# Kernel optimization log

Hardware: AMD Instinct MI355X
Metric: run time of the kernel (lower is better)

The kernel has to match this reference:

```python
import jax, jax.numpy as jnp
import numpy as np
from jax import lax

# channel-gather index lists for the 16 c3 branches (from the torch source)
IDX3 = np.array([0,1,2, 1,2,3, 2,3,4, 3,4,5, 0,4,5, 0,1,5])          # 6 branches x 3 ch
IDX4 = np.array([0,1,2,3, 1,2,3,4, 2,3,4,5, 0,3,4,5, 0,1,4,5,
                 0,1,2,5, 0,1,3,4, 1,2,4,5, 0,2,3,5])                  # 9 branches x 4 ch
F6_SCALE = 1.7519


def _conv(x, w, groups=1):
    # NCHW x OIHW, stride 1, VALID padding (all convs in the model)
    return lax.conv_general_dilated(x, w, (1, 1), 'VALID', feature_group_count=groups)


def _avgpool2(x):
    return lax.reduce_window(x, 0.0, lax.add, (1, 1, 2, 2), (1, 1, 2, 2), 'VALID') * 0.25


def _bconv(x, w, b, groups=1):
    # BinaryConvFunction.forward: sign(conv(sign(x), sign(w)) + b)
    out = _conv(jnp.sign(x), jnp.sign(w), groups) + b[None, :, None, None]
    return jnp.sign(out)


def setup_inputs() -> dict:
    key = jax.random.key(0)
    ks = jax.random.split(key, 16)
    B = 8192
    return {
        'x':     jax.random.normal(ks[0], (B, 1, 32, 32), jnp.float32),
        'c1_w':  jax.random.normal(ks[1], (6, 1, 5, 5), jnp.float32) * 0.2,
        'c1_b':  jax.random.normal(ks[2], (6,), jnp.float32) * 0.1,
        'w3':    jax.random.normal(ks[3], (6, 3, 5, 5), jnp.float32),   # 6 grouped 3-ch branches
        'b3':    jax.random.normal(ks[4], (6,), jnp.float32) * 0.1,
        'w4':    jax.random.normal(ks[5], (9, 4, 5, 5), jnp.float32),   # 9 grouped 4-ch branches
        'b4':    jax.random.normal(ks[6], (9,), jnp.float32) * 0.1,
        'w6':    jax.random.normal(ks[7], (1, 6, 5, 5), jnp.float32),   # 1 branch on all 6 ch
        'b6':    jax.random.normal(ks[8], (1,), jnp.float32) * 0.1,
        'c5_w':  jax.random.normal(ks[9], (120, 16, 5, 5), jnp.float32),
        'c5_b':  jax.random.normal(ks[10], (120,), jnp.float32) * 0.1,
        'f6_w':  jax.random.normal(ks[11], (84, 120), jnp.float32) * 0.1,
        'f6_b':  jax.random.normal(ks[12], (84,), jnp.float32) * 0.1,
        'rbf_w': jax.random.normal(ks[13], (10, 84), jnp.float32) * 0.1,
        'rbf_b': jax.random.normal(ks[14], (10,), jnp.float32) * 0.1,
    }


def reference(x, c1_w, c1_b, w3, b3, w4, b4, w6, b6, c5_w, c5_b, f6_w, f6_b, rbf_w, rbf_b):
    # c1 (full-precision conv) + relu + s2 avgpool: [B,1,32,32] -> [B,6,14,14]
    h = _avgpool2(jax.nn.relu(_conv(x, c1_w) + c1_b[None, :, None, None]))
    # 16 binary branch convs, batched as grouped convs over gathered channels
    o3 = _bconv(h[:, IDX3], w3, b3, groups=6)   # [B,6,10,10]
    o4 = _bconv(h[:, IDX4], w4, b4, groups=9)   # [B,9,10,10]
    o6 = _bconv(h, w6, b6)                      # [B,1,10,10]
    h = jnp.concatenate([o3, o4, o6], axis=1)   # [B,16,10,10] (matches torch cat order)
    h = _avgpool2(jax.nn.relu(h))               # [B,16,5,5]
    h = _bconv(h, c5_w, c5_b)                   # [B,120,1,1]
    h = h.reshape(h.shape[0], -1)               # [B,120]
    h = jnp.tanh((h @ f6_w.T + f6_b) * F6_SCALE)
    return jax.nn.relu(h @ rbf_w.T + rbf_b)     # [B,10]
```

## Files before the change

kernel.cpp:

```cpp
#include <hip/hip_runtime.h>
#include <stdint.h>

typedef float v2f __attribute__((ext_vector_type(2)));

constexpr int IDX3[18] = {0,1,2, 1,2,3, 2,3,4, 3,4,5, 0,4,5, 0,1,5};
constexpr int IDX4[36] = {0,1,2,3, 1,2,3,4, 2,3,4,5, 0,3,4,5, 0,1,4,5,
                          0,1,2,5, 0,1,3,4, 1,2,4,5, 0,2,3,5};


__global__ void prepack_kernel(const float* __restrict__ w3, const float* __restrict__ w4,
                               const float* __restrict__ w6, const float* __restrict__ c5w,
                               unsigned* __restrict__ ws) {
    int t = blockIdx.x * blockDim.x + threadIdx.x;
    if (t < 60) {
        const float* src = (t < 18) ? (w3 + t * 25)
                          : (t < 54) ? (w4 + (t - 18) * 25)
                          : (w6 + (t - 54) * 25);
        unsigned m = 0;
        for (int p = 0; p < 25; ++p) if (src[p] > 0.f) m |= 1u << p;
        ws[t] = m;
    } else if (t < 1620) {
        int q = t - 60, oc = q / 13, w = q % 13;
        unsigned m = 0;
        for (int b = 0; b < 32; ++b) {
            int g = w * 32 + b;
            int qi = g >> 4, ic = g & 15;
            if (qi < 25 && c5w[oc * 400 + ic * 25 + qi] > 0.f) m |= 1u << b;
        }
        ws[60 + q] = m;
    }
}

__global__ __launch_bounds__(256, 4) void lenet_fused(
    const float* __restrict__ x, const float* __restrict__ c1w, const float* __restrict__ c1b,
    const float* __restrict__ b3, const float* __restrict__ b4, const float* __restrict__ b6,
    const float* __restrict__ c5b, const unsigned* __restrict__ ws,
    const float* __restrict__ f6w, const float* __restrict__ f6b,
    const float* __restrict__ rbfw, const float* __restrict__ rbfb,
    float* __restrict__ out, int B) {
    __shared__ float wS[150];
    __shared__ float bS[6], b3S[6], b4S[9], b6S[1];
    __shared__ unsigned hrow[3][6][14];
    __shared__ unsigned sbits[3][100];
    __shared__ unsigned c5in[3][13];
    __shared__ float4 sS4[3][30];
    __shared__ float f6o[3][84];

    const int t = threadIdx.x;
    const int img0 = blockIdx.x * 3;
    const int nimg = min(3, B - img0);

    if (t < 150) wS[t] = c1w[t];
    if (t < 6) { bS[t] = c1b[t]; b3S[t] = b3[t]; }
    if (t < 9) b4S[t] = b4[t];
    if (t == 0) b6S[0] = b6[0];
    __syncthreads();

    if (t < nimg * 84) {
        const int denom = nimg * 6;
        int py = t / denom, rem = t % denom, img = rem / 6, c = rem % 6;
        float wr[25];
        #pragma unroll
        for (int i = 0; i < 25; ++i) wr[i] = wS[c * 25 + i];
        const float bias = bS[c];
        v2f accp[28];
        #pragma unroll
        for (int j = 0; j < 28; ++j) accp[j] = (v2f){bias, bias};
        const float* xp = x + (size_t)(img0 + img) * 1024 + (2 * py) * 32;
        #pragma unroll
        for (int r = 0; r < 6; ++r) {
            float rv[32];
            #pragma unroll
            for (int q = 0; q < 8; ++q) {
                float4 v = ((const float4*)(xp + r * 32))[q];
                rv[4 * q] = v.x; rv[4 * q + 1] = v.y; rv[4 * q + 2] = v.z; rv[4 * q + 3] = v.w;
            }
            if (r == 0) {
                #pragma unroll
                for (int kw = 0; kw < 5; ++kw) {
                    float wv = wr[kw];
                    #pragma unroll
                    for (int cx = 0; cx < 28; ++cx)
                        accp[cx].x = fmaf(rv[cx + kw], wv, accp[cx].x);
                }
            } else if (r == 5) {
                #pragma unroll
                for (int kw = 0; kw < 5; ++kw) {
                    float wv = wr[20 + kw];
                    #pragma unroll
                    for (int cx = 0; cx < 28; ++cx)
                        accp[cx].y = fmaf(rv[cx + kw], wv, accp[cx].y);
                }
            } else {
                v2f wp[5];
                #pragma unroll
                for (int kw = 0; kw < 5; ++kw)
                    wp[kw] = (v2f){wr[r * 5 + kw], wr[(r - 1) * 5 + kw]};
                #pragma unroll
                for (int kw = 0; kw < 5; ++kw) {
                    v2f w2 = wp[kw];
                    #pragma unroll
                    for (int cx = 0; cx < 28; ++cx) {
                        v2f x2 = (v2f){rv[cx + kw], rv[cx + kw]};
                        accp[cx] = x2 * w2 + accp[cx];
                    }
                }
            }
        }
        unsigned m = 0;
        #pragma unroll
        for (int px = 0; px < 14; ++px) {
            float mx = fmaxf(fmaxf(accp[2 * px].x, accp[2 * px].y),
                             fmaxf(accp[2 * px + 1].x, accp[2 * px + 1].y));
            if (mx > 0.f) m |= 1u << px;
        }
        hrow[img][c][py] = m;
    }
    __syncthreads();

    for (int q = t; q < nimg * 100; q += 256) {
        int img = q / 100, p = q % 100, oy = p / 10, ox = p % 10;
        unsigned win[6];
        int wpop[6];
        #pragma unroll
        for (int c = 0; c < 6; ++c) {
            unsigned w = 0;
            #pragma unroll
            for (int r = 0; r < 5; ++r)
                w |= ((hrow[img][c][oy + r] >> ox) & 31u) << (5 * r);
            win[c] = w;
            wpop[c] = __popc(w);
        }
        unsigned m16 = 0;
        #pragma unroll
        for (int br = 0; br < 6; ++br) {
            int sum = 0, tot = 0;
            #pragma unroll
            for (int j = 0; j < 3; ++j) {
                int c = IDX3[br * 3 + j];
                tot += wpop[c];
                sum += __popc(win[c] & ws[br * 3 + j]);
            }
            if ((float)(2 * sum - tot) + b3S[br] > 0.f) m16 |= 1u << br;
        }
        #pragma unroll
        for (int br = 0; br < 9; ++br) {
            int sum = 0, tot = 0;
            #pragma unroll
            for (int j = 0; j < 4; ++j) {
                int c = IDX4[br * 4 + j];
                tot += wpop[c];
                sum += __popc(win[c] & ws[18 + br * 4 + j]);
            }
            if ((float)(2 * sum - tot) + b4S[br] > 0.f) m16 |= 1u << (6 + br);
        }
        {
            int sum = 0, tot = 0;
            #pragma unroll
            for (int c = 0; c < 6; ++c) {
                tot += wpop[c];
                sum += __popc(win[c] & ws[54 + c]);
            }
            if ((float)(2 * sum - tot) + b6S[0] > 0.f) m16 |= 1u << 15;
        }
        sbits[img][p] = m16;
    }
    __syncthreads();

    for (int q = t; q < nimg * 13; q += 256) {
        int img = q / 13, j = q % 13;
        int qi0 = 2 * j;
        int qy = qi0 / 5, qx = qi0 % 5, base = 2 * qy * 10 + 2 * qx;
        unsigned a0 = sbits[img][base] | sbits[img][base + 1] |
                      sbits[img][base + 10] | sbits[img][base + 11];
        unsigned word = a0 & 0xFFFFu;
        if (j < 12) {
            int qi1 = qi0 + 1;
            qy = qi1 / 5; qx = qi1 % 5; base = 2 * qy * 10 + 2 * qx;
            unsigned a1 = sbits[img][base] | sbits[img][base + 1] |
                          sbits[img][base + 10] | sbits[img][base + 11];
            word |= (a1 & 0xFFFFu) << 16;
        }
        c5in[img][j] = word;
    }
    __syncthreads();

    for (int q = t; q < nimg * 120; q += 256) {
        int img = q / 120, oc = q % 120;
        const unsigned* cm = ws + 60 + oc * 13;
        int sum = 0, tot = 0;
        #pragma unroll
        for (int w = 0; w < 13; ++w) {
            unsigned inw = c5in[img][w];
            tot += __popc(inw);
            sum += __popc(inw & cm[w]);
        }
        bool pos = ((float)(2 * sum - tot) + c5b[oc]) > 0.f;
        ((float*)sS4)[img * 120 + oc] = pos ? 1.f : -1.f;
    }
    __syncthreads();

    if (t < nimg * 84) {
        int img = t / 84, j = t % 84;
        float acc = f6b[j];
        const float4* wrow = (const float4*)f6w + j * 30;
        #pragma unroll 6
        for (int kk = 0; kk < 30; ++kk) {
            float4 wv = wrow[kk];
            float4 sv = sS4[img][kk];
            acc = fmaf(sv.x, wv.x, acc);
            acc = fmaf(sv.y, wv.y, acc);
            acc = fmaf(sv.z, wv.z, acc);
            acc = fmaf(sv.w, wv.w, acc);
        }
        f6o[img][j] = tanhf(1.7519f * acc);
    }
    __syncthreads();

    if (t < nimg * 10) {
        int img = t / 10, oc = t % 10;
        float sum = rbfb[oc];
        const float4* rw = (const float4*)(rbfw + oc * 84);
        #pragma unroll
        for (int kk = 0; kk < 21; ++kk) {
            float4 wv = rw[kk];
            int j = 4 * kk;
            sum = fmaf(f6o[img][j + 0], wv.x, sum);
            sum = fmaf(f6o[img][j + 1], wv.y, sum);
            sum = fmaf(f6o[img][j + 2], wv.z, sum);
            sum = fmaf(f6o[img][j + 3], wv.w, sum);
        }
        out[(size_t)(img0 + img) * 10 + oc] = fmaxf(sum, 0.f);
    }
}

extern "C" void kernel_launch(void* const* d_in, const int* in_sizes, int n_in,
                              void* d_out, int out_size, void* d_ws, size_t ws_size,
                              hipStream_t stream) {
    const float* x    = (const float*)d_in[0];
    const float* c1w  = (const float*)d_in[1];
    const float* c1b  = (const float*)d_in[2];
    const float* w3   = (const float*)d_in[3];
    const float* b3   = (const float*)d_in[4];
    const float* w4   = (const float*)d_in[5];
    const float* b4   = (const float*)d_in[6];
    const float* w6   = (const float*)d_in[7];
    const float* b6   = (const float*)d_in[8];
    const float* c5w  = (const float*)d_in[9];
    const float* c5b  = (const float*)d_in[10];
    const float* f6w  = (const float*)d_in[11];
    const float* f6b  = (const float*)d_in[12];
    const float* rbfw = (const float*)d_in[13];
    const float* rbfb = (const float*)d_in[14];
    const int B = in_sizes[0] / 1024;

    unsigned* ws = (unsigned*)d_ws;

    prepack_kernel<<<dim3(7), dim3(256), 0, stream>>>(w3, w4, w6, c5w, ws);
    lenet_fused<<<dim3((B + 2) / 3), dim3(256), 0, stream>>>(
        x, c1w, c1b, b3, b4, b6, c5b, ws, f6w, f6b, rbfw, rbfb, (float*)d_out, B);
}
```

Before: 153.1 us.

## Split c1 stage into its own fully-occupied kernel writing 16-bit row masks

Moves the full-precision c1 conv, relu and pool into a separate kernel where every thread computes one (image, row, channel) mask, so all 256 lanes are busy rather than only 252 of them with long idle tails in the fused kernel. The weight prepacking is folded into the first blocks of that kernel, removing one launch. The tail kernel now reads the packed 16-bit masks from workspace. This adds a global round trip and an extra launch boundary, and relies on the tail kernel seeing the prepacked weights only after the first kernel finishes.

Result: slower. 162.0 us (+5.8%).

```diff
diff --git a/kernel.cpp b/kernel.cpp
--- a/kernel.cpp
+++ b/kernel.cpp
@@ -8,38 +8,108 @@
                           0,1,2,5, 0,1,3,4, 1,2,4,5, 0,2,3,5};
 
 
-__global__ void prepack_kernel(const float* __restrict__ w3, const float* __restrict__ w4,
-                               const float* __restrict__ w6, const float* __restrict__ c5w,
-                               unsigned* __restrict__ ws) {
-    int t = blockIdx.x * blockDim.x + threadIdx.x;
-    if (t < 60) {
-        const float* src = (t < 18) ? (w3 + t * 25)
-                          : (t < 54) ? (w4 + (t - 18) * 25)
-                          : (w6 + (t - 54) * 25);
-        unsigned m = 0;
-        for (int p = 0; p < 25; ++p) if (src[p] > 0.f) m |= 1u << p;
-        ws[t] = m;
-    } else if (t < 1620) {
-        int q = t - 60, oc = q / 13, w = q % 13;
-        unsigned m = 0;
-        for (int b = 0; b < 32; ++b) {
-            int g = w * 32 + b;
-            int qi = g >> 4, ic = g & 15;
-            if (qi < 25 && c5w[oc * 400 + ic * 25 + qi] > 0.f) m |= 1u << b;
-        }
-        ws[60 + q] = m;
-    }
+__global__ __launch_bounds__(256) void k_c1(
+    const float* __restrict__ x, const float* __restrict__ c1w, const float* __restrict__ c1b,
+    const float* __restrict__ w3, const float* __restrict__ w4, const float* __restrict__ w6,
+    const float* __restrict__ c5w, unsigned* __restrict__ ws, int B) {
+    __shared__ float wS[150];
+    __shared__ float bS[6];
+
+    const int t = threadIdx.x;
+    if (t < 150) wS[t] = c1w[t];
+    if (t < 6) bS[t] = c1b[t];
+
+    if (blockIdx.x < 7) {
+        int pt = blockIdx.x * 256 + t;
+        if (pt < 60) {
+            const float* src = (pt < 18) ? (w3 + pt * 25)
+                              : (pt < 54) ? (w4 + (pt - 18) * 25)
+                              : (w6 + (pt - 54) * 25);
+            unsigned m = 0;
+            for (int p = 0; p < 25; ++p) if (src[p] > 0.f) m |= 1u << p;
+            ws[pt] = m;
+        } else if (pt < 1620) {
+            int q = pt - 60, oc = q / 13, w = q % 13;
+            unsigned m = 0;
+            for (int b = 0; b < 32; ++b) {
+                int g = w * 32 + b;
+                int qi = g >> 4, ic = g & 15;
+                if (qi < 25 && c5w[oc * 400 + ic * 25 + qi] > 0.f) m |= 1u << b;
+            }
+            ws[60 + q] = m;
+        }
+    }
+    __syncthreads();
+
+    const int tid = blockIdx.x * 256 + t;
+    if (tid >= B * 84) return;
+    const int img = tid / 84, r84 = tid % 84, py = r84 / 6, c = r84 % 6;
+
+    float wr[25];
+    #pragma unroll
+    for (int i = 0; i < 25; ++i) wr[i] = wS[c * 25 + i];
+    const float bias = bS[c];
+    v2f accp[28];
+    #pragma unroll
+    for (int j = 0; j < 28; ++j) accp[j] = (v2f){bias, bias};
+    const float* xp = x + (size_t)img * 1024 + (2 * py) * 32;
+    #pragma unroll
+    for (int r = 0; r < 6; ++r) {
+        float rv[32];
+        #pragma unroll
+        for (int q = 0; q < 8; ++q) {
+            float4 v = ((const float4*)(xp + r * 32))[q];
+            rv[4 * q] = v.x; rv[4 * q + 1] = v.y; rv[4 * q + 2] = v.z; rv[4 * q + 3] = v.w;
+        }
+        if (r == 0) {
+            #pragma unroll
+            for (int kw = 0; kw < 5; ++kw) {
+                float wv = wr[kw];
+                #pragma unroll
+                for (int cx = 0; cx < 28; ++cx)
+                    accp[cx].x = fmaf(rv[cx + kw], wv, accp[cx].x);
+            }
+        } else if (r == 5) {
+            #pragma unroll
+            for (int kw = 0; kw < 5; ++kw) {
+                float wv = wr[20 + kw];
+                #pragma unroll
+                for (int cx = 0; cx < 28; ++cx)
+                    accp[cx].y = fmaf(rv[cx + kw], wv, accp[cx].y);
+            }
+        } else {
+            v2f wp[5];
+            #pragma unroll
+            for (int kw = 0; kw < 5; ++kw)
+                wp[kw] = (v2f){wr[r * 5 + kw], wr[(r - 1) * 5 + kw]};
+            #pragma unroll
+            for (int kw = 0; kw < 5; ++kw) {
+                v2f w2 = wp[kw];
+                #pragma unroll
+                for (int cx = 0; cx < 28; ++cx) {
+                    v2f x2 = (v2f){rv[cx + kw], rv[cx + kw]};
+                    accp[cx] = x2 * w2 + accp[cx];
+                }
+            }
+        }
+    }
+    unsigned m = 0;
+    #pragma unroll
+    for (int px = 0; px < 14; ++px) {
+        float mx = fmaxf(fmaxf(accp[2 * px].x, accp[2 * px].y),
+                         fmaxf(accp[2 * px + 1].x, accp[2 * px + 1].y));
+        if (mx > 0.f) m |= 1u << px;
+    }
+    ((unsigned short*)(ws + 1620))[tid] = (unsigned short)m;
 }
 
-__global__ __launch_bounds__(256, 4) void lenet_fused(
-    const float* __restrict__ x, const float* __restrict__ c1w, const float* __restrict__ c1b,
+__global__ __launch_bounds__(256) void k_tail(
     const float* __restrict__ b3, const float* __restrict__ b4, const float* __restrict__ b6,
     const float* __restrict__ c5b, const unsigned* __restrict__ ws,
     const float* __restrict__ f6w, const float* __restrict__ f6b,
     const float* __restrict__ rbfw, const float* __restrict__ rbfb,
     float* __restrict__ out, int B) {
-    __shared__ float wS[150];
-    __shared__ float bS[6], b3S[6], b4S[9], b6S[1];
+    __shared__ float b3S[6], b4S[9], b6S[1];
     __shared__ unsigned hrow[3][6][14];
     __shared__ unsigned sbits[3][100];
     __shared__ unsigned c5in[3][13];
@@ -50,72 +120,16 @@
     const int img0 = blockIdx.x * 3;
     const int nimg = min(3, B - img0);
 
-    if (t < 150) wS[t] = c1w[t];
-    if (t < 6) { bS[t] = c1b[t]; b3S[t] = b3[t]; }
+    {
+        const unsigned short* h16 = (const unsigned short*)(ws + 1620) + img0 * 84;
+        if (t < nimg * 84) {
+            int img = t / 84, rr = t % 84, py = rr / 6, c = rr % 6;
+            hrow[img][c][py] = h16[t];
+        }
+    }
+    if (t < 6) b3S[t] = b3[t];
     if (t < 9) b4S[t] = b4[t];
     if (t == 0) b6S[0] = b6[0];
-    __syncthreads();
-
-    if (t < nimg * 84) {
-        const int denom = nimg * 6;
-        int py = t / denom, rem = t % denom, img = rem / 6, c = rem % 6;
-        float wr[25];
-        #pragma unroll
-        for (int i = 0; i < 25; ++i) wr[i] = wS[c * 25 + i];
-        const float bias = bS[c];
-        v2f accp[28];
-        #pragma unroll
-        for (int j = 0; j < 28; ++j) accp[j] = (v2f){bias, bias};
-        const float* xp = x + (size_t)(img0 + img) * 1024 + (2 * py) * 32;
-        #pragma unroll
-        for (int r = 0; r < 6; ++r) {
-            float rv[32];
-            #pragma unroll
-            for (int q = 0; q < 8; ++q) {
-                float4 v = ((const float4*)(xp + r * 32))[q];
-                rv[4 * q] = v.x; rv[4 * q + 1] = v.y; rv[4 * q + 2] = v.z; rv[4 * q + 3] = v.w;
-            }
-            if (r == 0) {
-                #pragma unroll
-                for (int kw = 0; kw < 5; ++kw) {
-                    float wv = wr[kw];
-                    #pragma unroll
-                    for (int cx = 0; cx < 28; ++cx)
-                        accp[cx].x = fmaf(rv[cx + kw], wv, accp[cx].x);
-                }
-            } else if (r == 5) {
-                #pragma unroll
-                for (int kw = 0; kw < 5; ++kw) {
-                    float wv = wr[20 + kw];
-                    #pragma unroll
-                    for (int cx = 0; cx < 28; ++cx)
-                        accp[cx].y = fmaf(rv[cx + kw], wv, accp[cx].y);
-                }
-            } else {
-                v2f wp[5];
-                #pragma unroll
-                for (int kw = 0; kw < 5; ++kw)
-                    wp[kw] = (v2f){wr[r * 5 + kw], wr[(r - 1) * 5 + kw]};
-                #pragma unroll
-                for (int kw = 0; kw < 5; ++kw) {
-                    v2f w2 = wp[kw];
-                    #pragma unroll
-                    for (int cx = 0; cx < 28; ++cx) {
-                        v2f x2 = (v2f){rv[cx + kw], rv[cx + kw]};
-                        accp[cx] = x2 * w2 + accp[cx];
-                    }
-                }
-            }
-        }
-        unsigned m = 0;
-        #pragma unroll
-        for (int px = 0; px < 14; ++px) {
-            float mx = fmaxf(fmaxf(accp[2 * px].x, accp[2 * px].y),
-                             fmaxf(accp[2 * px + 1].x, accp[2 * px + 1].y));
-            if (mx > 0.f) m |= 1u << px;
-        }
-        hrow[img][c][py] = m;
-    }
     __syncthreads();
 
     for (int q = t; q < nimg * 100; q += 256) {
@@ -256,7 +270,8 @@
 
     unsigned* ws = (unsigned*)d_ws;
 
-    prepack_kernel<<<dim3(7), dim3(256), 0, stream>>>(w3, w4, w6, c5w, ws);
-    lenet_fused<<<dim3((B + 2) / 3), dim3(256), 0, stream>>>(
-        x, c1w, c1b, b3, b4, b6, c5b, ws, f6w, f6b, rbfw, rbfb, (float*)d_out, B);
+    k_c1<<<dim3((B * 84 + 255) / 256), dim3(256), 0, stream>>>(
+        x, c1w, c1b, w3, w4, w6, c5w, ws, B);
+    k_tail<<<dim3((B + 2) / 3), dim3(256), 0, stream>>>(
+        b3, b4, b6, c5b, ws, f6w, f6b, rbfw, rbfb, (float*)d_out, B);
 }
```
